# Optimization experiments

Measured on AMD Instinct MI355X. Metric: run time of the kernel, lower is better.

The kernel has to match this reference:

```python
import jax, jax.numpy as jnp
import numpy as np

N, F_IN, H, C = 8192, 1024, 512, 64

def setup_inputs() -> dict:
    key = jax.random.key(0)
    k1, k2, k3, k4, k5, k6 = jax.random.split(key, 6)
    X = jax.random.normal(k1, (N, F_IN), dtype=jnp.float32)
    tilde = jax.random.uniform(k2, (N, N), dtype=jnp.float32)
    # torch.nn.Linear params, stored as [in, out] for direct matmul
    W1 = jax.random.normal(k3, (F_IN, H), dtype=jnp.float32) * (1.0 / np.sqrt(F_IN))
    b1 = jax.random.normal(k4, (H,), dtype=jnp.float32) * 0.01
    W2 = jax.random.normal(k5, (H, C), dtype=jnp.float32) * (1.0 / np.sqrt(H))
    b2 = jax.random.normal(k6, (C,), dtype=jnp.float32) * 0.01
    return {"X": X, "tilde": tilde, "W1": W1, "b1": b1, "W2": W2, "b2": b2}

def reference(X, tilde, W1, b1, W2, b2):
    # normalize(): D1 = col sums, D2 = row sums; torch broadcasting applies
    # BOTH [N] vectors over the column axis: A[i,j] = sqrt(D1[j])*tilde[i,j]*sqrt(D2[j])
    D1 = jnp.sum(tilde, axis=0)  # [N]
    D2 = jnp.sum(tilde, axis=1)  # [N]
    scale = jnp.sqrt(D1) * jnp.sqrt(D2)  # [N], column scaling
    A = tilde * scale[None, :]  # [N, N] normalized adjacency
    # Layer 1: Linear then propagate, ReLU
    h = jax.nn.relu(A @ (X @ W1 + b1))  # [N, H]
    # Layer 2: Linear then propagate
    out = A @ (h @ W2 + b2)  # [N, C]
    return out
```

## Files before the change

kernel.cpp:

```cpp
#include <hip/hip_runtime.h>
#include <hip/hip_bf16.h>
#include <cstdint>
#include <cstddef>

typedef __attribute__((ext_vector_type(8))) __bf16 bf16x8;
typedef __attribute__((ext_vector_type(4))) float f32x4;
typedef __attribute__((ext_vector_type(4))) unsigned short u16x4;

#define DEVINL static __device__ __forceinline__

DEVINL unsigned short f2bf(float x) {
  union { float f; unsigned u; } un; un.f = x;
  unsigned r = un.u + 0x7fffu + ((un.u >> 16) & 1u);
  return (unsigned short)(r >> 16);
}

DEVINL float bf2f(unsigned short b) {
  union { unsigned u; float f; } un; un.u = ((unsigned)b) << 16;
  return un.f;
}

DEVINL void gload16(const void* g, void* l) {
  __builtin_amdgcn_global_load_lds(
      (__attribute__((address_space(1))) void*)(void*)(uintptr_t)(const void*)g,
      (__attribute__((address_space(3))) void*)l, 16, 0, 0);
}

#define SBAR() asm volatile("s_barrier" ::: "memory")
#define WLG0() asm volatile("s_waitcnt lgkmcnt(0)" ::: "memory")
#define WVM6() asm volatile("s_waitcnt vmcnt(6)" ::: "memory")

__global__ __launch_bounds__(256, 4) void sums_convert(const float* __restrict__ tilde,
                                                       float4* __restrict__ partials4,
                                                       float* __restrict__ D2,
                                                       u16x4* __restrict__ Tbf) {
  const int t = threadIdx.x;
  float4 ca[8];
#pragma unroll
  for (int i = 0; i < 8; ++i) ca[i] = (float4){0.f, 0.f, 0.f, 0.f};
  float rs[8];
#pragma unroll
  for (int r = 0; r < 8; ++r) rs[r] = 0.f;

  const int base_row = blockIdx.x * 8;
#pragma unroll
  for (int r = 0; r < 8; ++r) {
    const size_t rowoff = (size_t)(base_row + r) * 2048;
    const float4* rp = (const float4*)tilde + rowoff;
    u16x4* op = Tbf + rowoff;
#pragma unroll
    for (int i = 0; i < 8; ++i) {
      float4 v = rp[t + i * 256];
      ca[i].x += v.x; ca[i].y += v.y; ca[i].z += v.z; ca[i].w += v.w;
      rs[r] += (v.x + v.y) + (v.z + v.w);
      u16x4 o;
      o[0] = f2bf(v.x); o[1] = f2bf(v.y); o[2] = f2bf(v.z); o[3] = f2bf(v.w);
      op[t + i * 256] = o;
    }
  }
  float4* pb = partials4 + (size_t)blockIdx.x * 2048;
#pragma unroll
  for (int i = 0; i < 8; ++i) pb[t + i * 256] = ca[i];

#pragma unroll
  for (int r = 0; r < 8; ++r) {
#pragma unroll
    for (int off = 32; off > 0; off >>= 1) rs[r] += __shfl_down(rs[r], off, 64);
  }
  __shared__ float wsum[4][8];
  const int wave = t >> 6;
  if ((t & 63) == 0) {
#pragma unroll
    for (int r = 0; r < 8; ++r) wsum[wave][r] = rs[r];
  }
  __syncthreads();
  if (t < 8) D2[base_row + t] = wsum[0][t] + wsum[1][t] + wsum[2][t] + wsum[3][t];
}

__global__ __launch_bounds__(256) void zreduce(const float4* __restrict__ partials4,
                                               float4* __restrict__ partials2_4) {
  const int c4 = blockIdx.x * 256 + threadIdx.x;
  const int z0 = blockIdx.y * 16;
  float4 s = (float4){0.f, 0.f, 0.f, 0.f};
#pragma unroll 4
  for (int z = z0; z < z0 + 16; ++z) {
    float4 v = partials4[(size_t)z * 2048 + c4];
    s.x += v.x; s.y += v.y; s.z += v.z; s.w += v.w;
  }
  partials2_4[(size_t)blockIdx.y * 2048 + c4] = s;
}

__global__ __launch_bounds__(256) void colscale_kernel(const float* __restrict__ partials2,
                                                       const float* __restrict__ D2,
                                                       float* __restrict__ sv) {
  int j = blockIdx.x * 256 + threadIdx.x;
  float d1 = 0.f;
  for (int z = 0; z < 64; ++z) d1 += partials2[z * 8192 + j];
  sv[j] = sqrtf(d1 * D2[j]);
}

__global__ __launch_bounds__(256) void convert_bf16(const float4* __restrict__ in,
                                                    u16x4* __restrict__ out, int n4) {
  const int stride = gridDim.x * 256;
  for (int i = blockIdx.x * 256 + threadIdx.x; i < n4; i += stride) {
    float4 v = in[i];
    u16x4 o;
    o[0] = f2bf(v.x); o[1] = f2bf(v.y); o[2] = f2bf(v.z); o[3] = f2bf(v.w);
    out[i] = o;
  }
}

__global__ __launch_bounds__(256) void transpose_cvt(const float* __restrict__ in,
                                                     unsigned short* __restrict__ out,
                                                     int R, int C) {
  int o = blockIdx.x * 256 + threadIdx.x;
  if (o >= R * C) return;
  int c = o / R, r = o - c * R;
  out[o] = f2bf(in[(size_t)r * C + c]);
}

__global__ __launch_bounds__(512, 2) void gemm2_8ph(
    const unsigned short* __restrict__ A,
    const unsigned short* __restrict__ BT,
    unsigned short* __restrict__ Cpart) {
  constexpr int K = 8192;
  constexpr int LDC = 512;
  constexpr int NT = 32;

  __shared__ __align__(16) char lds[131072];

  const int tid = threadIdx.x;
  const int lane = tid & 63, w = tid >> 6;
  const int wr = w >> 2, wc = w & 3;
  const int lrow = lane & 15, slot = lane >> 4;
  const int xorv = (((lrow >> 2) & 1) << 5) | (((lrow >> 3) & 1) << 6);
  const int row0 = blockIdx.x * 256;
  const int col0 = blockIdx.y * 256;
  const size_t kbeg = (size_t)blockIdx.z * 2048;

  f32x4 acc[8][4];
#pragma unroll
  for (int m = 0; m < 8; ++m)
#pragma unroll
    for (int n = 0; n < 4; ++n) acc[m][n] = (f32x4){0.f, 0.f, 0.f, 0.f};
  bf16x8 a[4][2], b[4][2];

  auto STAGE_A = [&](int buf, int h, int tk) {
    if (tk >= NT) return;
    const size_t kabs = kbeg + (size_t)tk * 64;
    char* dst = lds + buf * 65536;
#pragma unroll
    for (int j = 0; j < 2; ++j) {
      int L = h * 16384 + (j * 512 + tid) * 16;
      int y = L ^ ((L & 0x600) >> 4);
      int lam = y >> 7, cb = y & 127;
      int R = ((lam >> 6) & 1) * 128 + (lam >> 7) * 64 + (lam & 63);
      gload16((const char*)A + ((size_t)(row0 + R) * K + kabs) * 2 + cb, dst + L);
    }
  };
  auto STAGE_B = [&](int buf, int h, int tk) {
    if (tk >= NT) return;
    const size_t kabs = kbeg + (size_t)tk * 64;
    char* dst = lds + buf * 65536 + 32768;
#pragma unroll
    for (int j = 0; j < 2; ++j) {
      int L = h * 16384 + (j * 512 + tid) * 16;
      int y = L ^ ((L & 0x600) >> 4);
      int lam = y >> 7, cb = y & 127;
      int R = ((lam >> 5) & 3) * 64 + (lam >> 7) * 32 + (lam & 31);
      gload16((const char*)BT + ((size_t)(col0 + R) * K + kabs) * 2 + cb, dst + L);
    }
  };
  auto LDA = [&](int buf, int mh) {
    const char* base = lds + buf * 65536;
#pragma unroll
    for (int mm = 0; mm < 4; ++mm)
#pragma unroll
      for (int ks = 0; ks < 2; ++ks) {
        int lin = mh * 16384 + wr * 8192 + mm * 2048 + lrow * 128 + ks * 64 + slot * 16;
        a[mm][ks] = *(const bf16x8*)(base + (lin ^ xorv));
      }
  };
  auto LDB = [&](int buf, int nh) {
    const char* base = lds + buf * 65536 + 32768;
#pragma unroll
    for (int nn = 0; nn < 2; ++nn)
#pragma unroll
      for (int ks = 0; ks < 2; ++ks) {
        int lin = nh * 16384 + wc * 4096 + nn * 2048 + lrow * 128 + ks * 64 + slot * 16;
        b[nh * 2 + nn][ks] = *(const bf16x8*)(base + (lin ^ xorv));
      }
  };
  auto MMA = [&](int mh, int nh) {
    __builtin_amdgcn_s_setprio(1);
#pragma unroll
    for (int mm = 0; mm < 4; ++mm)
#pragma unroll
      for (int nn = 0; nn < 2; ++nn)
#pragma unroll
        for (int ks = 0; ks < 2; ++ks)
          acc[mh * 4 + mm][nh * 2 + nn] = __builtin_amdgcn_mfma_f32_16x16x32_bf16(
              a[mm][ks], b[nh * 2 + nn][ks], acc[mh * 4 + mm][nh * 2 + nn], 0, 0, 0);
    __builtin_amdgcn_s_setprio(0);
  };

  STAGE_A(0, 0, 0); STAGE_B(0, 0, 0); STAGE_B(0, 1, 0); STAGE_A(0, 1, 0);
  STAGE_A(1, 0, 1); STAGE_B(1, 0, 1); STAGE_B(1, 1, 1);
  WVM6(); SBAR();

  for (int it = 0; it < NT / 2; ++it) {
    const int t = 2 * it;
    LDA(0, 0); LDB(0, 0);
    STAGE_A(1, 1, t + 1);
    SBAR(); WLG0();
    MMA(0, 0);
    SBAR();
    LDB(0, 1);
    STAGE_A(0, 0, t + 2);
    SBAR(); WLG0();
    MMA(0, 1);
    SBAR();
    LDA(0, 1);
    STAGE_B(0, 0, t + 2);
    SBAR(); WLG0();
    MMA(1, 1);
    SBAR();
    STAGE_B(0, 1, t + 2);
    WVM6();
    SBAR();
    MMA(1, 0);
    SBAR();
    LDA(1, 0); LDB(1, 0);
    STAGE_A(0, 1, t + 2);
    SBAR(); WLG0();
    MMA(0, 0);
    SBAR();
    LDB(1, 1);
    STAGE_A(1, 0, t + 3);
    SBAR(); WLG0();
    MMA(0, 1);
    SBAR();
    LDA(1, 1);
    STAGE_B(1, 0, t + 3);
    SBAR(); WLG0();
    MMA(1, 1);
    SBAR();
    STAGE_B(1, 1, t + 3);
    WVM6();
    SBAR();
    MMA(1, 0);
    SBAR();
  }

  unsigned short* Cb = Cpart + (size_t)blockIdx.z * 8192 * LDC;
  const int r0 = row0 + wr * 128, c0 = col0 + wc * 64;
#pragma unroll
  for (int m = 0; m < 8; ++m)
#pragma unroll
    for (int n = 0; n < 4; ++n)
#pragma unroll
      for (int j = 0; j < 4; ++j) {
        int row = r0 + m * 16 + (lane >> 4) * 4 + j;
        int col = c0 + n * 16 + lrow;
        Cb[(size_t)row * LDC + col] = f2bf(acc[m][n][j]);
      }
}

template <int BM, int BN, int EPI>
__global__ __launch_bounds__(256) void gemm_bt(
    const unsigned short* __restrict__ A,
    const unsigned short* __restrict__ BT,
    void* __restrict__ C,
    const float* __restrict__ bias,
    const float* __restrict__ cs,
    int M, int N, int K, int kChunk, int ldc) {
  constexpr int WTM = BM / 2, WTN = BN / 2;
  constexpr int MR = WTM / 16, NR = WTN / 16;
  constexpr int AIT = BM * 4 / 256;
  constexpr int BIT = BN * 4 / 256;

  __shared__ unsigned short As[BM * 32];
  __shared__ unsigned short Bs[BN * 32];

  const int t = threadIdx.x;
  const int lane = t & 63, wave = t >> 6;
  const int wr = wave >> 1, wc = wave & 1;
  const int bm = blockIdx.x, bn = blockIdx.y, bz = blockIdx.z;
  const int row0 = bm * BM, col0 = bn * BN;
  const int kbeg = bz * kChunk, kend = kbeg + kChunk;
  const int lrow = lane & 15;
  const int lk = (lane >> 4) * 8;

  f32x4 acc[MR][NR];
#pragma unroll
  for (int m = 0; m < MR; ++m)
#pragma unroll
    for (int n = 0; n < NR; ++n) acc[m][n] = (f32x4){0.f, 0.f, 0.f, 0.f};

  for (int k0 = kbeg; k0 < kend; k0 += 32) {
#pragma unroll
    for (int i = 0; i < AIT; ++i) {
      int flat = i * 256 + t;
      int r = flat >> 2, ko = (flat & 3) * 8;
      gload16(A + (size_t)(row0 + r) * K + k0 + ko, As + (size_t)flat * 8);
    }
#pragma unroll
    for (int i = 0; i < BIT; ++i) {
      int flat = i * 256 + t;
      int r = flat >> 2, ko = (flat & 3) * 8;
      gload16(BT + (size_t)(col0 + r) * K + k0 + ko, Bs + (size_t)flat * 8);
    }
    __syncthreads();

    bf16x8 af[MR], bfr[NR];
#pragma unroll
    for (int m = 0; m < MR; ++m)
      af[m] = *(const bf16x8*)&As[(wr * WTM + m * 16 + lrow) * 32 + lk];
#pragma unroll
    for (int n = 0; n < NR; ++n)
      bfr[n] = *(const bf16x8*)&Bs[(wc * WTN + n * 16 + lrow) * 32 + lk];
#pragma unroll
    for (int m = 0; m < MR; ++m)
#pragma unroll
      for (int n = 0; n < NR; ++n)
        acc[m][n] = __builtin_amdgcn_mfma_f32_16x16x32_bf16(af[m], bfr[n], acc[m][n], 0, 0, 0);
    __syncthreads();
  }

  const int r0 = row0 + wr * WTM, c0 = col0 + wc * WTN;
  if constexpr (EPI == 2) {
    float* Cf = (float*)C + (size_t)bz * M * ldc;
#pragma unroll
    for (int m = 0; m < MR; ++m)
#pragma unroll
      for (int n = 0; n < NR; ++n)
#pragma unroll
        for (int j = 0; j < 4; ++j) {
          int row = r0 + m * 16 + (lane >> 4) * 4 + j;
          int col = c0 + n * 16 + lrow;
          Cf[(size_t)row * ldc + col] = acc[m][n][j];
        }
  } else if constexpr (EPI == 4) {
    unsigned short* Cb = (unsigned short*)C + (size_t)bz * M * ldc;
#pragma unroll
    for (int m = 0; m < MR; ++m)
#pragma unroll
      for (int n = 0; n < NR; ++n)
#pragma unroll
        for (int j = 0; j < 4; ++j) {
          int row = r0 + m * 16 + (lane >> 4) * 4 + j;
          int col = c0 + n * 16 + lrow;
          Cb[(size_t)row * ldc + col] = f2bf(acc[m][n][j]);
        }
  } else {
    unsigned short* Cb = (unsigned short*)C;
#pragma unroll
    for (int m = 0; m < MR; ++m)
#pragma unroll
      for (int n = 0; n < NR; ++n)
#pragma unroll
        for (int j = 0; j < 4; ++j) {
          int row = r0 + m * 16 + (lane >> 4) * 4 + j;
          int col = c0 + n * 16 + lrow;
          float v = acc[m][n][j];
          if constexpr (EPI == 1) v = v > 0.f ? v : 0.f;
          if constexpr (EPI == 3) v = (v + bias[row]) * cs[col];
          Cb[(size_t)row * ldc + col] = f2bf(v);
        }
  }
}

__global__ __launch_bounds__(256) void reduce_relu_b16p(const u16x4* __restrict__ part,
                                                        u16x4* __restrict__ out,
                                                        int total4, int splits) {
  const int stride = gridDim.x * 256;
  for (int i = blockIdx.x * 256 + threadIdx.x; i < total4; i += stride) {
    float s0 = 0.f, s1 = 0.f, s2 = 0.f, s3 = 0.f;
    for (int z = 0; z < splits; ++z) {
      u16x4 v = part[(size_t)z * total4 + i];
      s0 += bf2f(v[0]); s1 += bf2f(v[1]); s2 += bf2f(v[2]); s3 += bf2f(v[3]);
    }
    u16x4 o;
    o[0] = f2bf(s0 > 0.f ? s0 : 0.f);
    o[1] = f2bf(s1 > 0.f ? s1 : 0.f);
    o[2] = f2bf(s2 > 0.f ? s2 : 0.f);
    o[3] = f2bf(s3 > 0.f ? s3 : 0.f);
    out[i] = o;
  }
}

__global__ __launch_bounds__(256) void reduce_zt(const float4* __restrict__ part,
                                                 const float* __restrict__ b2,
                                                 const float* __restrict__ sv,
                                                 u16x4* __restrict__ out) {
  const int i4 = blockIdx.x * 256 + threadIdx.x;
  const int row = i4 >> 11;
  const int col0 = (i4 & 2047) * 4;
  float4 s = part[i4];
#pragma unroll
  for (int z = 1; z < 4; ++z) {
    float4 v = part[(size_t)z * 131072 + i4];
    s.x += v.x; s.y += v.y; s.z += v.z; s.w += v.w;
  }
  const float b = b2[row];
  u16x4 o;
  o[0] = f2bf((s.x + b) * sv[col0 + 0]);
  o[1] = f2bf((s.y + b) * sv[col0 + 1]);
  o[2] = f2bf((s.z + b) * sv[col0 + 2]);
  o[3] = f2bf((s.w + b) * sv[col0 + 3]);
  out[i4] = o;
}

__global__ __launch_bounds__(256) void reduce_out(const u16x4* __restrict__ part,
                                                  float4* __restrict__ out,
                                                  int total4, int splits) {
  const int i = blockIdx.x * 256 + threadIdx.x;
  if (i >= total4) return;
  float s0 = 0.f, s1 = 0.f, s2 = 0.f, s3 = 0.f;
  for (int z = 0; z < splits; ++z) {
    u16x4 v = part[(size_t)z * total4 + i];
    s0 += bf2f(v[0]); s1 += bf2f(v[1]); s2 += bf2f(v[2]); s3 += bf2f(v[3]);
  }
  out[i] = (float4){s0, s1, s2, s3};
}

extern "C" void kernel_launch(void* const* d_in, const int* in_sizes, int n_in,
                              void* d_out, int out_size, void* d_ws, size_t ws_size,
                              hipStream_t stream) {
  const float* X     = (const float*)d_in[0];
  const float* tilde = (const float*)d_in[1];
  const float* W1    = (const float*)d_in[2];
  const float* b1    = (const float*)d_in[3];
  const float* W2    = (const float*)d_in[4];
  const float* b2    = (const float*)d_in[5];
  float* out = (float*)d_out;

  constexpr int N = 8192, F = 1024, H = 512, Cc = 64;

  char* ws = (char*)d_ws;
  size_t off = 0;
  auto alloc = [&](size_t bytes) {
    char* p = ws + off;
    off += (bytes + 255) & ~(size_t)255;
    return p;
  };
  unsigned short* Tbf  = (unsigned short*)alloc((size_t)N * N * 2);
  unsigned short* XW1T = (unsigned short*)alloc((size_t)H * N * 2);
  unsigned short* hbuf = (unsigned short*)alloc((size_t)N * H * 2);
  unsigned short* ZT   = (unsigned short*)alloc((size_t)Cc * N * 2);
  unsigned short* W2T  = (unsigned short*)alloc((size_t)Cc * H * 2);
  float* partials2 = (float*)alloc(64 * N * 4);
  float* D2 = (float*)alloc(N * 4);
  float* sv = (float*)alloc(N * 4);
  const size_t scratch_base = off;
  unsigned short* Xbf = (unsigned short*)(ws + scratch_base);
  unsigned short* W1T = (unsigned short*)(ws + scratch_base + (size_t)N * F * 2);
  float* partials = (float*)(ws + scratch_base + (size_t)N * F * 2 + 0x200000);
  unsigned short* part2 = (unsigned short*)(ws + scratch_base);
  float* part3 = (float*)(ws + scratch_base);
  unsigned short* part4 = (unsigned short*)(ws + scratch_base);

  const size_t need_split = scratch_base + (size_t)N * F * 2 + 0x200000 + (size_t)1024 * N * 4;
  const bool splitk = ws_size >= need_split;

  sums_convert<<<1024, 256, 0, stream>>>(tilde, (float4*)partials, D2, (u16x4*)Tbf);
  zreduce<<<dim3(8, 64), 256, 0, stream>>>((const float4*)partials, (float4*)partials2);
  colscale_kernel<<<N / 256, 256, 0, stream>>>(partials2, D2, sv);

  convert_bf16<<<2048, 256, 0, stream>>>((const float4*)X, (u16x4*)Xbf, N * F / 4);
  transpose_cvt<<<(F * H) / 256, 256, 0, stream>>>(W1, W1T, F, H);
  transpose_cvt<<<(H * Cc) / 256, 256, 0, stream>>>(W2, W2T, H, Cc);

  gemm_bt<64, 128, 3><<<dim3(H / 64, N / 128, 1), 256, 0, stream>>>(
      W1T, Xbf, XW1T, b1, sv, H, N, F, F, N);

  if (splitk) {
    gemm2_8ph<<<dim3(N / 256, H / 256, 4), 512, 0, stream>>>(Tbf, XW1T, part2);
    reduce_relu_b16p<<<1024, 256, 0, stream>>>((const u16x4*)part2, (u16x4*)hbuf,
                                               N * H / 4, 4);
    gemm_bt<64, 128, 2><<<dim3(1, N / 128, 4), 256, 0, stream>>>(
        W2T, hbuf, part3, nullptr, nullptr, Cc, N, H, H / 4, N);
    reduce_zt<<<(Cc * N / 4) / 256, 256, 0, stream>>>((const float4*)part3, b2, sv,
                                                      (u16x4*)ZT);
    gemm_bt<128, 64, 4><<<dim3(N / 128, 1, 16), 256, 0, stream>>>(
        Tbf, ZT, part4, nullptr, nullptr, N, Cc, N, N / 16, Cc);
    reduce_out<<<(N * Cc / 4) / 256, 256, 0, stream>>>((const u16x4*)part4, (float4*)out,
                                                       N * Cc / 4, 16);
  } else {
    gemm_bt<128, 128, 1><<<dim3(N / 128, H / 128, 1), 256, 0, stream>>>(
        Tbf, XW1T, hbuf, nullptr, nullptr, N, H, N, N, H);
    gemm_bt<64, 128, 3><<<dim3(1, N / 128, 1), 256, 0, stream>>>(
        W2T, hbuf, ZT, b2, sv, Cc, N, H, H, N);
    gemm_bt<128, 64, 4><<<dim3(N / 128, 1, 1), 256, 0, stream>>>(
        Tbf, ZT, part4, nullptr, nullptr, N, Cc, N, N, Cc);
    reduce_out<<<(N * Cc / 4) / 256, 256, 0, stream>>>((const u16x4*)part4, (float4*)out,
                                                       N * Cc / 4, 1);
  }
}
```

Measured before the change: 270.4 us.

## Fuse prep conversions, double rows per sums block, halve final split-K

The three input-conversion kernels (X to bf16, W1 and W2 transpose-convert) are merged into one launch with block ranges for each job. sums_convert now processes 16 rows per block, which halves the partial column-sum buffer and the zreduce work per slice. The last A@Z GEMM drops from 16 to 8 K-splits, so the partial-output reduce is smaller. Each is meant to cut launch overhead and partial-sum traffic, at the cost of fewer blocks and less parallelism in the sums and final GEMM stages.

```diff
diff --git a/kernel.cpp b/kernel.cpp
--- a/kernel.cpp
+++ b/kernel.cpp
@@ -30,7 +30,7 @@
 #define WLG0() asm volatile("s_waitcnt lgkmcnt(0)" ::: "memory")
 #define WVM6() asm volatile("s_waitcnt vmcnt(6)" ::: "memory")
 
-__global__ __launch_bounds__(256, 4) void sums_convert(const float* __restrict__ tilde,
+__global__ __launch_bounds__(256, 2) void sums_convert(const float* __restrict__ tilde,
                                                        float4* __restrict__ partials4,
                                                        float* __restrict__ D2,
                                                        u16x4* __restrict__ Tbf) {
@@ -38,13 +38,12 @@
   float4 ca[8];
 #pragma unroll
   for (int i = 0; i < 8; ++i) ca[i] = (float4){0.f, 0.f, 0.f, 0.f};
-  float rs[8];
-#pragma unroll
-  for (int r = 0; r < 8; ++r) rs[r] = 0.f;
-
-  const int base_row = blockIdx.x * 8;
-#pragma unroll
-  for (int r = 0; r < 8; ++r) {
+  float rs[16];
+#pragma unroll
+  for (int r = 0; r < 16; ++r) rs[r] = 0.f;
+
+  const int base_row = blockIdx.x * 16;
+  for (int r = 0; r < 16; ++r) {
     const size_t rowoff = (size_t)(base_row + r) * 2048;
     const float4* rp = (const float4*)tilde + rowoff;
     u16x4* op = Tbf + rowoff;
@@ -63,27 +62,27 @@
   for (int i = 0; i < 8; ++i) pb[t + i * 256] = ca[i];
 
 #pragma unroll
-  for (int r = 0; r < 8; ++r) {
+  for (int r = 0; r < 16; ++r) {
 #pragma unroll
     for (int off = 32; off > 0; off >>= 1) rs[r] += __shfl_down(rs[r], off, 64);
   }
-  __shared__ float wsum[4][8];
+  __shared__ float wsum[4][16];
   const int wave = t >> 6;
   if ((t & 63) == 0) {
 #pragma unroll
-    for (int r = 0; r < 8; ++r) wsum[wave][r] = rs[r];
+    for (int r = 0; r < 16; ++r) wsum[wave][r] = rs[r];
   }
   __syncthreads();
-  if (t < 8) D2[base_row + t] = wsum[0][t] + wsum[1][t] + wsum[2][t] + wsum[3][t];
+  if (t < 16) D2[base_row + t] = wsum[0][t] + wsum[1][t] + wsum[2][t] + wsum[3][t];
 }
 
 __global__ __launch_bounds__(256) void zreduce(const float4* __restrict__ partials4,
                                                float4* __restrict__ partials2_4) {
   const int c4 = blockIdx.x * 256 + threadIdx.x;
-  const int z0 = blockIdx.y * 16;
+  const int z0 = blockIdx.y * 8;
   float4 s = (float4){0.f, 0.f, 0.f, 0.f};
-#pragma unroll 4
-  for (int z = z0; z < z0 + 16; ++z) {
+#pragma unroll
+  for (int z = z0; z < z0 + 8; ++z) {
     float4 v = partials4[(size_t)z * 2048 + c4];
     s.x += v.x; s.y += v.y; s.z += v.z; s.w += v.w;
   }
@@ -99,24 +98,30 @@
   sv[j] = sqrtf(d1 * D2[j]);
 }
 
-__global__ __launch_bounds__(256) void convert_bf16(const float4* __restrict__ in,
-                                                    u16x4* __restrict__ out, int n4) {
-  const int stride = gridDim.x * 256;
-  for (int i = blockIdx.x * 256 + threadIdx.x; i < n4; i += stride) {
-    float4 v = in[i];
-    u16x4 o;
-    o[0] = f2bf(v.x); o[1] = f2bf(v.y); o[2] = f2bf(v.z); o[3] = f2bf(v.w);
-    out[i] = o;
-  }
-}
-
-__global__ __launch_bounds__(256) void transpose_cvt(const float* __restrict__ in,
-                                                     unsigned short* __restrict__ out,
-                                                     int R, int C) {
-  int o = blockIdx.x * 256 + threadIdx.x;
-  if (o >= R * C) return;
-  int c = o / R, r = o - c * R;
-  out[o] = f2bf(in[(size_t)r * C + c]);
+__global__ __launch_bounds__(256) void prep_fused(const float4* __restrict__ X4,
+                                                  u16x4* __restrict__ Xbf4,
+                                                  const float* __restrict__ W1,
+                                                  unsigned short* __restrict__ W1T,
+                                                  const float* __restrict__ W2,
+                                                  unsigned short* __restrict__ W2T) {
+  const int b = blockIdx.x;
+  if (b < 2048) {
+    const int n4 = 8192 * 1024 / 4;
+    for (int i = b * 256 + threadIdx.x; i < n4; i += 2048 * 256) {
+      float4 v = X4[i];
+      u16x4 o;
+      o[0] = f2bf(v.x); o[1] = f2bf(v.y); o[2] = f2bf(v.z); o[3] = f2bf(v.w);
+      Xbf4[i] = o;
+    }
+  } else if (b < 4096) {
+    int o = (b - 2048) * 256 + threadIdx.x;
+    int c = o >> 10, r = o & 1023;
+    W1T[o] = f2bf(W1[(size_t)r * 512 + c]);
+  } else {
+    int o = (b - 4096) * 256 + threadIdx.x;
+    int c = o >> 9, r = o & 511;
+    W2T[o] = f2bf(W2[(size_t)r * 64 + c]);
+  }
 }
 
 __global__ __launch_bounds__(512, 2) void gemm2_8ph(
@@ -460,16 +465,15 @@
   float* part3 = (float*)(ws + scratch_base);
   unsigned short* part4 = (unsigned short*)(ws + scratch_base);
 
-  const size_t need_split = scratch_base + (size_t)N * F * 2 + 0x200000 + (size_t)1024 * N * 4;
+  const size_t need_split =
+      scratch_base + (size_t)N * F * 2 + 0x200000 + (size_t)512 * N * 4;
   const bool splitk = ws_size >= need_split;
 
-  sums_convert<<<1024, 256, 0, stream>>>(tilde, (float4*)partials, D2, (u16x4*)Tbf);
+  sums_convert<<<512, 256, 0, stream>>>(tilde, (float4*)partials, D2, (u16x4*)Tbf);
   zreduce<<<dim3(8, 64), 256, 0, stream>>>((const float4*)partials, (float4*)partials2);
   colscale_kernel<<<N / 256, 256, 0, stream>>>(partials2, D2, sv);
 
-  convert_bf16<<<2048, 256, 0, stream>>>((const float4*)X, (u16x4*)Xbf, N * F / 4);
-  transpose_cvt<<<(F * H) / 256, 256, 0, stream>>>(W1, W1T, F, H);
-  transpose_cvt<<<(H * Cc) / 256, 256, 0, stream>>>(W2, W2T, H, Cc);
+  prep_fused<<<4224, 256, 0, stream>>>((const float4*)X, (u16x4*)Xbf, W1, W1T, W2, W2T);
 
   gemm_bt<64, 128, 3><<<dim3(H / 64, N / 128, 1), 256, 0, stream>>>(
       W1T, Xbf, XW1T, b1, sv, H, N, F, F, N);
@@ -482,10 +486,10 @@
         W2T, hbuf, part3, nullptr, nullptr, Cc, N, H, H / 4, N);
     reduce_zt<<<(Cc * N / 4) / 256, 256, 0, stream>>>((const float4*)part3, b2, sv,
                                                       (u16x4*)ZT);
-    gemm_bt<128, 64, 4><<<dim3(N / 128, 1, 16), 256, 0, stream>>>(
-        Tbf, ZT, part4, nullptr, nullptr, N, Cc, N, N / 16, Cc);
+    gemm_bt<128, 64, 4><<<dim3(N / 128, 1, 8), 256, 0, stream>>>(
+        Tbf, ZT, part4, nullptr, nullptr, N, Cc, N, N / 8, Cc);
     reduce_out<<<(N * Cc / 4) / 256, 256, 0, stream>>>((const u16x4*)part4, (float4*)out,
-                                                       N * Cc / 4, 16);
+                                                       N * Cc / 4, 8);
   } else {
     gemm_bt<128, 128, 1><<<dim3(N / 128, H / 128, 1), 256, 0, stream>>>(
         Tbf, XW1T, hbuf, nullptr, nullptr, N, H, N, N, H);
```

After: 259.9 us. 3.9% less time.
